# Kernel optimization log

Hardware: AMD Instinct MI355X
Metric: run time of the kernel (lower is better)

Reference implementation:

```python
import jax, jax.numpy as jnp
import numpy as np

B, N, C, H = 32, 384, 768, 12
EPS = 1e-6

def setup_inputs() -> dict:
    key = jax.random.key(0)
    k0, k1, k2, k3 = jax.random.split(key, 4)
    x = jax.random.normal(k0, (B, N, C), dtype=jnp.float32)
    # binary keep-mask over key tokens, broadcastable to [B,1,N,N]
    policy = (jax.random.uniform(k1, (B, 1, 1, N)) > 0.5).astype(jnp.float32)
    qkv_w = jax.random.normal(k2, (3 * C, C), dtype=jnp.float32) * 0.02
    qkv_b = jnp.zeros((3 * C,), dtype=jnp.float32)
    proj_w = jax.random.normal(k3, (C, C), dtype=jnp.float32) * 0.02
    proj_b = jnp.zeros((C,), dtype=jnp.float32)
    return {"x": x, "policy": policy, "qkv_w": qkv_w, "qkv_b": qkv_b,
            "proj_w": proj_w, "proj_b": proj_b}

def reference(x, policy, qkv_w, qkv_b, proj_w, proj_b):
    b, n, c = x.shape
    hd = c // H
    scale = hd ** -0.5
    qkv = (x @ qkv_w.T + qkv_b).reshape(b, n, 3, H, hd).transpose(2, 0, 3, 1, 4)
    q, k, v = qkv[0], qkv[1], qkv[2]
    attn = jnp.einsum('bhnd,bhmd->bhnm', q, k) * scale  # [B,H,N,N]
    # softmax_with_policy: eye-blend so every token attends to itself,
    # then eps-regularized masked softmax
    eye = jnp.eye(n, dtype=policy.dtype)[None, None]  # [1,1,N,N]
    attn_policy = policy + (1.0 - policy) * eye       # broadcast -> [B,1,N,N]
    max_att = attn.max(axis=-1, keepdims=True)
    e = jnp.exp(attn - max_att) * attn_policy
    attn = (e + EPS / n) / (e.sum(axis=-1, keepdims=True) + EPS)
    out = jnp.einsum('bhnm,bhmd->bnhd', attn, v).reshape(b, n, c)
    return out @ proj_w.T + proj_b
```

## Files before the change

kernel.cpp:

```cpp
#include <hip/hip_runtime.h>

#define BB 32
#define NN 384
#define CC 768
#define HH 12
#define HD 64

typedef __attribute__((ext_vector_type(4))) float f32x4;
typedef __attribute__((ext_vector_type(8))) __bf16 bf16x8;
typedef __attribute__((ext_vector_type(4))) __bf16 bf16x4;

static __device__ __forceinline__ f32x4 mfma16(bf16x8 a, bf16x8 b, f32x4 c) {
    return __builtin_amdgcn_mfma_f32_16x16x32_bf16(a, b, c, 0, 0, 0);
}

static __device__ __forceinline__ void gload_lds16(const void* g, void* l) {
    __builtin_amdgcn_global_load_lds((const __attribute__((address_space(1))) void*)g,
                                     (__attribute__((address_space(3))) void*)l, 16, 0, 0);
}

#define XU   1179648
#define QU   73728
#define QKVU 221184
#define PU   73728
__global__ void cvt_kernel(const float* __restrict__ x, const float* __restrict__ qkv_w,
                           const float* __restrict__ proj_w, __bf16* __restrict__ dst) {
    const int i = blockIdx.x * blockDim.x + threadIdx.x;
    if (i >= XU + QKVU + PU) return;
    const float* src;
    float sc = 1.f;
    if (i < XU) src = x + (size_t)i * 8;
    else if (i < XU + QKVU) {
        src = qkv_w + (size_t)(i - XU) * 8;
        if (i < XU + QU) sc = 0.125f;
    } else src = proj_w + (size_t)(i - XU - QKVU) * 8;
    f32x4 a = *(const f32x4*)src;
    f32x4 b = *(const f32x4*)(src + 4);
    bf16x8 o;
#pragma unroll
    for (int j = 0; j < 4; ++j) { o[j] = (__bf16)(a[j] * sc); o[j + 4] = (__bf16)(b[j] * sc); }
    *(bf16x8*)(dst + (size_t)i * 8) = o;
}

template <int EPI>
__global__ __launch_bounds__(256, 2) void gemm_kernel(
    const __bf16* __restrict__ A, const __bf16* __restrict__ Bw,
    const float* __restrict__ bias,
    __bf16* __restrict__ qkbuf, __bf16* __restrict__ vtbuf,
    float* __restrict__ fout) {
    __shared__ __bf16 SA[2][128 * 64];
    __shared__ __bf16 SB[2][128 * 64];

    const int tid = threadIdx.x;
    const int l = tid & 63;
    const int w = tid >> 6;
    const int g = l >> 4, q16 = l & 15;
    const int mb = blockIdx.x * 128;
    const int nb = blockIdx.y * 128;
    const int wrb = (w >> 1) * 64;
    const int wcb = (w & 1) * 64;
    const int swz = q16 & 7;

    auto stage = [&](int buf, int kt) {
#pragma unroll
        for (int j = 0; j < 4; ++j) {
            const int ci = j * 256 + w * 64 + l;
            const int row = ci >> 3, c = ci & 7;
            const size_t go = (size_t)row * CC + kt * 64 + ((c ^ (row & 7)) << 3);
            gload_lds16(&A[(size_t)mb * CC + go], &SA[buf][(j * 256 + w * 64) * 8]);
            gload_lds16(&Bw[(size_t)nb * CC + go], &SB[buf][(j * 256 + w * 64) * 8]);
        }
    };

    f32x4 acc[4][4] = {};

    stage(0, 0);
    __syncthreads();

    for (int kt = 0; kt < 12; ++kt) {
        const int buf = kt & 1;
        if (kt < 11) stage(buf ^ 1, kt + 1);
        const char* pa = (const char*)&SA[buf][0];
        const char* pb = (const char*)&SB[buf][0];
#pragma unroll
        for (int c4 = 0; c4 < 2; ++c4) {
            bf16x8 af[4], bfr[4];
#pragma unroll
            for (int m = 0; m < 4; ++m)
                af[m] = *(const bf16x8*)(pa + (wrb + m * 16 + q16) * 128 +
                                         (((c4 * 4 + g) ^ swz) << 4));
#pragma unroll
            for (int n = 0; n < 4; ++n)
                bfr[n] = *(const bf16x8*)(pb + (wcb + n * 16 + q16) * 128 +
                                          (((c4 * 4 + g) ^ swz) << 4));
            __builtin_amdgcn_s_setprio(1);
#pragma unroll
            for (int m = 0; m < 4; ++m)
#pragma unroll
                for (int n = 0; n < 4; ++n)
                    acc[m][n] = mfma16(af[m], bfr[n], acc[m][n]);
            __builtin_amdgcn_s_setprio(0);
        }
        __syncthreads();
    }

    if constexpr (EPI == 0) {
        const int bbatch = mb / NN;
        const int tokb = mb % NN;
#pragma unroll
        for (int n = 0; n < 4; ++n) {
            const int colb = nb + wcb + n * 16;
            const int col = colb + q16;
            float bs = bias[col];
            if (colb < 2 * CC) {
                if (colb < CC) bs *= 0.125f;
#pragma unroll
                for (int m = 0; m < 4; ++m) {
                    const int row = mb + wrb + m * 16 + g * 4;
#pragma unroll
                    for (int r = 0; r < 4; ++r)
                        qkbuf[(size_t)(row + r) * 1536 + col] = (__bf16)(acc[m][n][r] + bs);
                }
            } else {
                const int dd = (col - 2 * CC) & 63;
                const int hh = (colb - 2 * CC) >> 6;
                __bf16* vp = vtbuf + ((size_t)(bbatch * HH + hh) * HD + dd) * NN;
#pragma unroll
                for (int m = 0; m < 4; ++m) {
                    const int tok = tokb + wrb + m * 16 + g * 4;
                    bf16x4 pk;
#pragma unroll
                    for (int r = 0; r < 4; ++r) pk[r] = (__bf16)(acc[m][n][r] + bs);
                    *(bf16x4*)&vp[tok] = pk;
                }
            }
        }
    } else {
#pragma unroll
        for (int n = 0; n < 4; ++n) {
            const int col = nb + wcb + n * 16 + q16;
            const float bs = bias[col];
#pragma unroll
            for (int m = 0; m < 4; ++m)
#pragma unroll
                for (int r = 0; r < 4; ++r)
                    fout[(size_t)(mb + wrb + m * 16 + g * 4 + r) * CC + col] = acc[m][n][r] + bs;
        }
    }
}

__global__ __launch_bounds__(512, 2) void attn_kernel(
    const __bf16* __restrict__ qkbuf, const __bf16* __restrict__ vtbuf,
    const float* __restrict__ policy, __bf16* __restrict__ attb) {
    __shared__ __bf16 Vlds[HD * NN];
    __shared__ float pol[NN];

    const int tid = threadIdx.x;
    const int l = tid & 63;
    const int w = tid >> 6;
    const int g = l >> 4, q16 = l & 15;
    const int bh = blockIdx.x;
    const int b = bh / HH, h = bh % HH;

    const __bf16* vg = vtbuf + (size_t)(b * HH + h) * HD * NN;
#pragma unroll
    for (int p = 0; p < 6; ++p) {
        const int cs = p * 512 + w * 64 + l;
        const int row = cs / 48, cin = cs - row * 48;
        gload_lds16(&vg[row * NN + ((cin ^ (row & 7)) << 3)], &Vlds[(p * 512 + w * 64) * 8]);
    }
    for (int i = tid; i < NN; i += 512) pol[i] = policy[b * NN + i];
    __syncthreads();

    const int sw = (q16 & 7) << 4;
    const __bf16* qg0 = qkbuf + (size_t)b * NN * 1536 + h * HD;
    const __bf16* kg = qg0 + CC;

    unsigned kw0 = 0, kw1 = 0, kw2 = 0;
#pragma unroll
    for (int kt = 0; kt < 6; ++kt)
#pragma unroll
        for (int t = 0; t < 4; ++t)
#pragma unroll
            for (int r = 0; r < 4; ++r) {
                const int key = kt * 64 + t * 16 + g * 4 + r;
                const unsigned bset = (pol[key] > 0.5f) ? 1u : 0u;
                const int bit = kt * 16 + t * 4 + r;
                if (bit < 32) kw0 |= bset << bit;
                else if (bit < 64) kw1 |= bset << (bit - 32);
                else kw2 |= bset << (bit - 64);
            }

#pragma unroll 1
    for (int ps = 0; ps < 3; ++ps) {
        const int qrow = ps * 128 + w * 16 + q16;
        const __bf16* qg = qg0 + (size_t)qrow * 1536;
        const bf16x8 qf0 = *(const bf16x8*)&qg[g * 8];
        const bf16x8 qf1 = *(const bf16x8*)&qg[32 + g * 8];

        unsigned pw0 = kw0, pw1 = kw1, pw2 = kw2;
        if (((qrow >> 2) & 3) == g) {
            const int sbit = (qrow >> 6) * 16 + ((qrow >> 4) & 3) * 4 + (qrow & 3);
            if (sbit < 32) pw0 |= 1u << sbit;
            else if (sbit < 64) pw1 |= 1u << (sbit - 32);
            else pw2 |= 1u << (sbit - 64);
        }

        f32x4 oacc[4] = {};
        f32x4 ssum = {0.f, 0.f, 0.f, 0.f};

#pragma unroll 2
        for (int kt = 0; kt < 6; ++kt) {
            f32x4 st[4];
            __builtin_amdgcn_s_setprio(1);
#pragma unroll
            for (int t = 0; t < 4; ++t) {
                const __bf16* kr = &kg[(size_t)((kt * 4 + t) * 16 + q16) * 1536];
                bf16x8 k0 = *(const bf16x8*)&kr[g * 8];
                bf16x8 k1 = *(const bf16x8*)&kr[32 + g * 8];
                f32x4 z = {0.f, 0.f, 0.f, 0.f};
                st[t] = mfma16(k1, qf1, mfma16(k0, qf0, z));
            }
            __builtin_amdgcn_s_setprio(0);

#pragma unroll
            for (int t = 0; t < 4; ++t) {
#pragma unroll
                for (int r = 0; r < 4; ++r) {
                    const int bit = kt * 16 + t * 4 + r;
                    const unsigned wsel = (bit < 32) ? pw0 : ((bit < 64) ? pw1 : pw2);
                    const bool keep = (wsel >> (bit & 31)) & 1u;
                    st[t][r] = keep ? __expf(st[t][r]) : 0.f;
                }
                ssum += st[t];
            }

            __builtin_amdgcn_s_setprio(1);
#pragma unroll
            for (int c4 = 0; c4 < 2; ++c4) {
                bf16x8 pf;
#pragma unroll
                for (int r = 0; r < 4; ++r) {
                    pf[r] = (__bf16)st[2 * c4][r];
                    pf[r + 4] = (__bf16)st[2 * c4 + 1][r];
                }
                const int c = kt * 2 + c4;
#pragma unroll
                for (int db = 0; db < 4; ++db) {
                    const int byte0 = (db * 16 + q16) * 768 + c * 64 + g * 8;
                    bf16x4 v0 = *(const bf16x4*)((const char*)Vlds + (byte0 ^ sw));
                    bf16x4 v1 = *(const bf16x4*)((const char*)Vlds + ((byte0 + 32) ^ sw));
                    bf16x8 vf;
#pragma unroll
                    for (int r = 0; r < 4; ++r) { vf[r] = v0[r]; vf[r + 4] = v1[r]; }
                    oacc[db] = mfma16(vf, pf, oacc[db]);
                }
            }
            __builtin_amdgcn_s_setprio(0);
        }

        float sum = (ssum[0] + ssum[1]) + (ssum[2] + ssum[3]);
        sum += __shfl_xor(sum, 16);
        sum += __shfl_xor(sum, 32);
        const float dinv = 1.f / (sum + 1e-6f);

        __bf16* op = attb + ((size_t)b * NN + qrow) * CC + h * HD;
#pragma unroll
        for (int db = 0; db < 4; ++db) {
            bf16x4 pk;
#pragma unroll
            for (int r = 0; r < 4; ++r) pk[r] = (__bf16)(oacc[db][r] * dinv);
            *(bf16x4*)&op[db * 16 + g * 4] = pk;
        }
    }
}

extern "C" void kernel_launch(void* const* d_in, const int* in_sizes, int n_in,
                              void* d_out, int out_size, void* d_ws, size_t ws_size,
                              hipStream_t stream) {
    (void)in_sizes; (void)n_in; (void)out_size; (void)ws_size;
    const float* x      = (const float*)d_in[0];
    const float* policy = (const float*)d_in[1];
    const float* qkv_w  = (const float*)d_in[2];
    const float* qkv_b  = (const float*)d_in[3];
    const float* proj_w = (const float*)d_in[4];
    const float* proj_b = (const float*)d_in[5];
    float* out = (float*)d_out;

    __bf16* xb    = (__bf16*)d_ws;
    __bf16* wqkv  = xb + (size_t)12288 * 768;
    __bf16* wproj = wqkv + (size_t)2304 * 768;
    __bf16* qkbuf = wproj + (size_t)768 * 768;
    __bf16* vtbuf = qkbuf + (size_t)12288 * 1536;
    __bf16* attb  = vtbuf + (size_t)BB * HH * HD * NN;

    const int units = XU + QKVU + PU;
    cvt_kernel<<<(units + 255) / 256, 256, 0, stream>>>(x, qkv_w, proj_w, xb);

    gemm_kernel<0><<<dim3(96, 18), 256, 0, stream>>>(xb, wqkv, qkv_b, qkbuf, vtbuf, nullptr);
    attn_kernel<<<384, 512, 0, stream>>>(qkbuf, vtbuf, policy, attb);
    gemm_kernel<1><<<dim3(96, 6), 256, 0, stream>>>(attb, wproj, proj_b, nullptr, nullptr, out);
}
```

Before: 168.9 us.

## Stage K in LDS and read V from pre-fragmented global layout

The QKV GEMM epilogue now writes V in an MFMA-fragment-ordered layout, so the attention kernel can load each lane's V operands with coalesced global reads. K is staged in swizzled LDS instead of being read row-strided from global memory. The launch bound rises to 4 blocks per CU, which fits because the shared buffer is the same size. This swaps which operand is reused from LDS and adds V global traffic inside the inner loop, traded against cheaper K access and higher occupancy.

```diff
diff --git a/kernel.cpp b/kernel.cpp
--- a/kernel.cpp
+++ b/kernel.cpp
@@ -124,14 +124,16 @@
             } else {
                 const int dd = (col - 2 * CC) & 63;
                 const int hh = (colb - 2 * CC) >> 6;
-                __bf16* vp = vtbuf + ((size_t)(bbatch * HH + hh) * HD + dd) * NN;
+                __bf16* vp = vtbuf + (size_t)(bbatch * HH + hh) * (HD * NN);
 #pragma unroll
                 for (int m = 0; m < 4; ++m) {
                     const int tok = tokb + wrb + m * 16 + g * 4;
+                    const int seg = (tok >> 5) * 8 + (((tok >> 4) & 1) << 2) + (dd >> 4);
+                    const int unit = ((tok >> 2) & 3) * 16 + (dd & 15);
                     bf16x4 pk;
 #pragma unroll
                     for (int r = 0; r < 4; ++r) pk[r] = (__bf16)(acc[m][n][r] + bs);
-                    *(bf16x4*)&vp[tok] = pk;
+                    *(bf16x4*)&vp[(seg * 64 + unit) * 4] = pk;
                 }
             }
         }
@@ -149,10 +151,10 @@
     }
 }
 
-__global__ __launch_bounds__(512, 2) void attn_kernel(
-    const __bf16* __restrict__ qkbuf, const __bf16* __restrict__ vtbuf,
+__global__ __launch_bounds__(512, 4) void attn_kernel(
+    const __bf16* __restrict__ qkbuf, const __bf16* __restrict__ vfrag,
     const float* __restrict__ policy, __bf16* __restrict__ attb) {
-    __shared__ __bf16 Vlds[HD * NN];
+    __shared__ __bf16 Klds[NN * HD];
     __shared__ float pol[NN];
 
     const int tid = threadIdx.x;
@@ -162,19 +164,20 @@
     const int bh = blockIdx.x;
     const int b = bh / HH, h = bh % HH;
 
-    const __bf16* vg = vtbuf + (size_t)(b * HH + h) * HD * NN;
+    const __bf16* kg = qkbuf + (size_t)b * NN * 1536 + CC + h * HD;
 #pragma unroll
     for (int p = 0; p < 6; ++p) {
         const int cs = p * 512 + w * 64 + l;
-        const int row = cs / 48, cin = cs - row * 48;
-        gload_lds16(&vg[row * NN + ((cin ^ (row & 7)) << 3)], &Vlds[(p * 512 + w * 64) * 8]);
+        const int row = cs >> 3, cin = cs & 7;
+        gload_lds16(&kg[(size_t)row * 1536 + (size_t)((cin ^ (row & 7)) << 3)],
+                    &Klds[(p * 512 + w * 64) * 8]);
     }
     for (int i = tid; i < NN; i += 512) pol[i] = policy[b * NN + i];
     __syncthreads();
 
     const int sw = (q16 & 7) << 4;
+    const __bf16* vfb = vfrag + (size_t)(b * HH + h) * (HD * NN);
     const __bf16* qg0 = qkbuf + (size_t)b * NN * 1536 + h * HD;
-    const __bf16* kg = qg0 + CC;
 
     unsigned kw0 = 0, kw1 = 0, kw2 = 0;
 #pragma unroll
@@ -193,7 +196,7 @@
 
 #pragma unroll 1
     for (int ps = 0; ps < 3; ++ps) {
-        const int qrow = ps * 128 + w * 16 + q16;
+        const int qrow = (ps * 8 + w) * 16 + q16;
         const __bf16* qg = qg0 + (size_t)qrow * 1536;
         const bf16x8 qf0 = *(const bf16x8*)&qg[g * 8];
         const bf16x8 qf1 = *(const bf16x8*)&qg[32 + g * 8];
@@ -215,13 +218,24 @@
             __builtin_amdgcn_s_setprio(1);
 #pragma unroll
             for (int t = 0; t < 4; ++t) {
-                const __bf16* kr = &kg[(size_t)((kt * 4 + t) * 16 + q16) * 1536];
-                bf16x8 k0 = *(const bf16x8*)&kr[g * 8];
-                bf16x8 k1 = *(const bf16x8*)&kr[32 + g * 8];
+                const int byte0 = ((kt * 4 + t) * 16 + q16) * 128 + g * 16;
+                bf16x8 k0 = *(const bf16x8*)((const char*)Klds + (byte0 ^ sw));
+                bf16x8 k1 = *(const bf16x8*)((const char*)Klds + ((byte0 + 64) ^ sw));
                 f32x4 z = {0.f, 0.f, 0.f, 0.f};
                 st[t] = mfma16(k1, qf1, mfma16(k0, qf0, z));
             }
             __builtin_amdgcn_s_setprio(0);
+
+            bf16x4 vv0[2][4], vv1[2][4];
+#pragma unroll
+            for (int c4 = 0; c4 < 2; ++c4) {
+                const int c = kt * 2 + c4;
+#pragma unroll
+                for (int db = 0; db < 4; ++db) {
+                    vv0[c4][db] = *(const bf16x4*)&vfb[((c * 8 + db) * 64 + l) * 4];
+                    vv1[c4][db] = *(const bf16x4*)&vfb[((c * 8 + 4 + db) * 64 + l) * 4];
+                }
+            }
 
 #pragma unroll
             for (int t = 0; t < 4; ++t) {
@@ -244,15 +258,14 @@
                     pf[r] = (__bf16)st[2 * c4][r];
                     pf[r + 4] = (__bf16)st[2 * c4 + 1][r];
                 }
-                const int c = kt * 2 + c4;
 #pragma unroll
                 for (int db = 0; db < 4; ++db) {
-                    const int byte0 = (db * 16 + q16) * 768 + c * 64 + g * 8;
-                    bf16x4 v0 = *(const bf16x4*)((const char*)Vlds + (byte0 ^ sw));
-                    bf16x4 v1 = *(const bf16x4*)((const char*)Vlds + ((byte0 + 32) ^ sw));
                     bf16x8 vf;
 #pragma unroll
-                    for (int r = 0; r < 4; ++r) { vf[r] = v0[r]; vf[r + 4] = v1[r]; }
+                    for (int r = 0; r < 4; ++r) {
+                        vf[r] = vv0[c4][db][r];
+                        vf[r + 4] = vv1[c4][db][r];
+                    }
                     oacc[db] = mfma16(vf, pf, oacc[db]);
                 }
             }
```

Result: faster. 139.8 us (-17.3%).
